# Kernel tuning notes

Hardware: AMD Instinct MI355X
Metric: run time of the kernel (lower is better)

The kernel has to match this reference:

```python
import jax, jax.numpy as jnp
import numpy as np
import math

FILT_LEN = 10  # all Farras / dual filters are 10-tap
INV_SQRT2 = 1.0 / math.sqrt(2.0)

# Farras first-stage analysis filters (fs_farras), shape [tree(2), lo/hi(2), 10]
_F = 0.08838834764832
_G = 0.01122679215254
_H = 0.69587998903400
FAF_NP = np.array([
    [[0.0, -_F, _F, _H, _H, _F, -_F, _G, _G, 0.0],
     [0.0, -_G, _G, _F, _F, -_H, _H, -_F, -_F, 0.0]],
    [[_G, _G, -_F, _F, _H, _H, _F, -_F, 0.0, 0.0],
     [0.0, 0.0, -_F, -_F, _H, -_H, _F, _F, _G, -_G]]], dtype=np.float32)
# Kingsbury Q-shift dual filters (duelfilt / dualfilt1), shape [tree(2), lo/hi(2), 10]
_A = 0.03516384
_B = 0.08832942
_C = 0.23389032
_D = 0.76027237
_E = 0.58751830
_K = 0.11430184
AF_NP = np.array([
    [[_A, 0.0, -_B, _C, _D, _E, 0.0, -_K, 0.0, 0.0],
     [0.0, 0.0, -_K, 0.0, _E, -_D, _C, _B, 0.0, -_A]],
    [[0.0, 0.0, -_K, 0.0, _E, _D, _C, -_B, 0.0, _A],
     [-_A, 0.0, _B, _C, -_D, _E, 0.0, -_K, 0.0, 0.0]]], dtype=np.float32)


def _afb_axis(x, lo_f, hi_f, axis):
    """1D circular analysis filter bank along spatial `axis` (1=rows, 2=cols).
    x: (B,H,W,C). Returns (lo, hi), each halved along `axis`.
    Math: x <- cshift(x,-L); y = downsample2(fullconv(x,f)); wrap-add first L taps.
    """
    N = x.shape[axis]
    L = FILT_LEN // 2
    C = x.shape[-1]
    x = jnp.roll(x, -L, axis=axis)

    def conv(f):
        kf = f[::-1].astype(x.dtype)  # lax does correlation -> flip for convolution
        if axis == 1:
            ker = jnp.tile(kf.reshape(FILT_LEN, 1, 1, 1), (1, 1, 1, C))
            pad = [(FILT_LEN - 1, FILT_LEN - 1), (0, 0)]
            strides = (2, 1)
        else:
            ker = jnp.tile(kf.reshape(1, FILT_LEN, 1, 1), (1, 1, 1, C))
            pad = [(0, 0), (FILT_LEN - 1, FILT_LEN - 1)]
            strides = (1, 2)
        return jax.lax.conv_general_dilated(
            x, ker, window_strides=strides, padding=pad,
            dimension_numbers=('NHWC', 'HWIO', 'NHWC'),
            feature_group_count=C)  # depthwise, per-channel identical filter

    def wrap(y):
        # y has N//2 + L samples along axis; fold periodic tail into head
        head = (jax.lax.slice_in_dim(y, 0, L, axis=axis)
                + jax.lax.slice_in_dim(y, N // 2, N // 2 + L, axis=axis))
        body = jax.lax.slice_in_dim(y, L, N // 2, axis=axis)
        return jnp.concatenate([head, body], axis=axis)

    return wrap(conv(lo_f)), wrap(conv(hi_f))


def afb2d(x, lo_row, hi_row, lo_col, hi_col):
    """2D separable analysis filter bank: returns (lo, [lohi, hilo, hihi])."""
    Lr, Hr = _afb_axis(x, lo_row, hi_row, axis=1)
    lo, w0 = _afb_axis(Lr, lo_col, hi_col, axis=2)
    w1, w2 = _afb_axis(Hr, lo_col, hi_col, axis=2)
    return lo, [w0, w1, w2]


def _add_sub(a, b):
    return (a + b) * INV_SQRT2, (a - b) * INV_SQRT2


def _dtcwt(x, Faf, af, level):
    x = x / 2
    w = [[[None, None] for _ in range(2)] for _ in range(level + 1)]
    for m in range(2):
        for n in range(2):
            lo, w[0][m][n] = afb2d(x, Faf[m, 0], Faf[m, 1], Faf[n, 0], Faf[n, 1])
            for j in range(1, level):
                lo, w[j][m][n] = afb2d(lo, af[m, 0], af[m, 1], af[n, 0], af[n, 1])
            w[level][m][n] = lo
    # combine dual trees into (approx) complex pairs
    for j in range(level):
        for s in range(3):
            w[j][0][0][s], w[j][1][1][s] = _add_sub(w[j][0][0][s], w[j][1][1][s])
            w[j][0][1][s], w[j][1][0][s] = _add_sub(w[j][0][1][s], w[j][1][0][s])
    # multiscale 2x2 tiling reassembly (concat=True path)
    wc = w
    for j in range(level - 1, 0, -1):
        for a in range(2):
            for b in range(2):
                wc[j][a][b] = jnp.concatenate([
                    jnp.concatenate([wc[j + 1][a][b], wc[j][a][b][0]], axis=2),
                    jnp.concatenate([wc[j][a][b][1], wc[j][a][b][2]], axis=2)], axis=1)
    tiles = []
    for a in range(2):
        for b in range(2):
            tiles.append(jnp.concatenate([
                jnp.concatenate([wc[1][a][b], wc[0][a][b][0]], axis=2),
                jnp.concatenate([wc[0][a][b][1], wc[0][a][b][2]], axis=2)], axis=1))
    w0, w1, w2, w3 = tiles
    return jnp.concatenate([jnp.concatenate([w0, w1], axis=2),
                            jnp.concatenate([w2, w3], axis=2)], axis=1)


def setup_inputs() -> dict:
    key = jax.random.key(0)
    x = jax.random.normal(key, (8, 512, 512, 3), dtype=jnp.float32)
    return {"x": x, "Faf": jnp.asarray(FAF_NP), "af": jnp.asarray(AF_NP), "level": 3}


def reference(x, Faf, af, level):
    return _dtcwt(x, Faf, af, int(level))
```

## Files before the change

kernel.cpp:

```cpp
#include <hip/hip_runtime.h>


#define FF 0.08838834764832f
#define GG 0.01122679215254f
#define HHc 0.69587998903400f
#define AAc 0.03516384f
#define BBc 0.08832942f
#define CCc 0.23389032f
#define DDc 0.76027237f
#define EEc 0.58751830f
#define KKc 0.11430184f

__device__ __constant__ float c_filt[2][2][2][10] = {
  {
    { {0.f,-FF, FF, HHc, HHc, FF,-FF, GG, GG, 0.f},
      {0.f,-GG, GG, FF, FF,-HHc, HHc,-FF,-FF, 0.f} },
    { {GG, GG,-FF, FF, HHc, HHc, FF,-FF, 0.f, 0.f},
      {0.f, 0.f,-FF,-FF, HHc,-HHc, FF, FF, GG,-GG} }
  },
  {
    { {AAc, 0.f,-BBc, CCc, DDc, EEc, 0.f,-KKc, 0.f, 0.f},
      {0.f, 0.f,-KKc, 0.f, EEc,-DDc, CCc, BBc, 0.f,-AAc} },
    { {0.f, 0.f,-KKc, 0.f, EEc, DDc, CCc,-BBc, 0.f, AAc},
      {-AAc, 0.f, BBc, CCc,-DDc, EEc, 0.f,-KKc, 0.f, 0.f} }
  }
};

__device__ __forceinline__ void cmb(float& a, float& b) {
  const float k = 0.70710678118654752440f;
  const float s = (a + b) * k, d = (a - b) * k;
  a = s; b = d;
}

__device__ __forceinline__ int swz4(int f4) { return f4 ^ ((f4 >> 3) & 7); }

template<int LVL, int N, int Ho, int Wo>
__global__ __launch_bounds__(256) void fused_level(
    const float* __restrict__ src,
    float* __restrict__ llout,
    float* __restrict__ out)
{
  constexpr int half = N / 2;
  constexpr int W2 = 2 * Wo + 8;
  constexpr int NF = (LVL == 0) ? 4 : 8;
  constexpr int ROWF = 3 * N;
  constexpr int FL = 3 * W2;
  constexpr int SIF4 = (3 * W2 * NF) / 4 + 4;
  constexpr size_t ZS = (size_t)8 * N * N * 3;
  constexpr size_t ZOUT = (size_t)8 * half * half * 3;
  __shared__ __align__(16) float inter[Ho * SIF4 * 4];

  const int jt = blockIdx.x, it = blockIdx.y, b = blockIdx.z;
  const int i0 = it * Ho, j0 = jt * Wo;
  const int tid = threadIdx.x;

  int base = (2 * j0 - 4) * 3;
  if (base < 0) base += ROWF;

  constexpr int I4 = FL / 4;
  for (int item = tid; item < Ho * I4; item += 256) {
    const int il = item / I4;
    const int q4 = (item - il * I4) * 4;
    int fg = base + q4;
    if (fg >= ROWF) fg -= ROWF;
    const int ig = i0 + il;
    float acc[NF][4];
#pragma unroll
    for (int f = 0; f < NF; ++f)
#pragma unroll
      for (int k = 0; k < 4; ++k) acc[f][k] = 0.f;

    if constexpr (LVL == 0) {
      const float* sp = src + (size_t)b * N * ROWF + fg;
#pragma unroll
      for (int t = 0; t < 10; ++t) {
        const int r = (2 * ig + 5 - t) & (N - 1);
        const float4 v = *(const float4*)(sp + (size_t)r * ROWF);
#pragma unroll
        for (int f = 0; f < 4; ++f) {
          const float fc = c_filt[0][f >> 1][f & 1][t];
          acc[f][0] += fc * v.x; acc[f][1] += fc * v.y;
          acc[f][2] += fc * v.z; acc[f][3] += fc * v.w;
        }
      }
#pragma unroll
      for (int f = 0; f < 4; ++f)
#pragma unroll
        for (int k = 0; k < 4; ++k) acc[f][k] *= 0.5f;
    } else {
#pragma unroll
      for (int z = 0; z < 4; ++z) {
        const int m = z >> 1;
        const float* sp = src + (size_t)z * ZS + (size_t)b * N * ROWF + fg;
#pragma unroll
        for (int t = 0; t < 10; ++t) {
          const int r = (2 * ig + 5 - t) & (N - 1);
          const float4 v = *(const float4*)(sp + (size_t)r * ROWF);
          const float fl = c_filt[1][m][0][t], fh = c_filt[1][m][1][t];
          acc[2 * z][0] += fl * v.x; acc[2 * z][1] += fl * v.y;
          acc[2 * z][2] += fl * v.z; acc[2 * z][3] += fl * v.w;
          acc[2 * z + 1][0] += fh * v.x; acc[2 * z + 1][1] += fh * v.y;
          acc[2 * z + 1][2] += fh * v.z; acc[2 * z + 1][3] += fh * v.w;
        }
      }
    }
#pragma unroll
    for (int k = 0; k < 4; ++k) {
      const int fq = q4 + k;
      if constexpr (NF == 4) {
        float4 w = make_float4(acc[0][k], acc[1][k], acc[2][k], acc[3][k]);
        *(float4*)&inter[(il * SIF4 + swz4(fq)) * 4] = w;
      } else {
        float4 w0 = make_float4(acc[0][k], acc[1][k], acc[2][k], acc[3][k]);
        float4 w1 = make_float4(acc[4][k], acc[5][k], acc[6][k], acc[7][k]);
        *(float4*)&inter[(il * SIF4 + swz4(2 * fq)) * 4] = w0;
        *(float4*)&inter[(il * SIF4 + swz4(2 * fq + 1)) * 4] = w1;
      }
    }
  }
  __syncthreads();

  if (tid < Ho * Wo) {
    const int il = tid / Wo, jl = tid - (tid / Wo) * Wo;
    float LL[4][3] = {}, LH[4][3] = {}, HL[4][3] = {}, HH[4][3] = {};
#pragma unroll
    for (int s = 0; s < 10; ++s) {
      const int wl = 2 * jl + 9 - s;
#pragma unroll
      for (int c = 0; c < 3; ++c) {
        if constexpr (LVL == 0) {
          const int f4 = wl * 3 + c;
          const float4 v = *(const float4*)&inter[(il * SIF4 + swz4(f4)) * 4];
          const float a0 = v.x, d0 = v.y, a1 = v.z, d1 = v.w;
#pragma unroll
          for (int n = 0; n < 2; ++n) {
            const float fl = c_filt[0][n][0][s], fh = c_filt[0][n][1][s];
            LL[n][c] += fl * a0; LH[n][c] += fh * a0;
            HL[n][c] += fl * d0; HH[n][c] += fh * d0;
            LL[2 + n][c] += fl * a1; LH[2 + n][c] += fh * a1;
            HL[2 + n][c] += fl * d1; HH[2 + n][c] += fh * d1;
          }
        } else {
          const int f4 = (wl * 3 + c) * 2;
          const float4 v0 = *(const float4*)&inter[(il * SIF4 + swz4(f4)) * 4];
          const float4 v1 = *(const float4*)&inter[(il * SIF4 + swz4(f4 + 1)) * 4];
          const float az[4] = {v0.x, v0.z, v1.x, v1.z};
          const float dz[4] = {v0.y, v0.w, v1.y, v1.w};
#pragma unroll
          for (int z = 0; z < 4; ++z) {
            const int n = z & 1;
            const float fl = c_filt[1][n][0][s], fh = c_filt[1][n][1][s];
            LL[z][c] += fl * az[z]; LH[z][c] += fh * az[z];
            HL[z][c] += fl * dz[z]; HH[z][c] += fh * dz[z];
          }
        }
      }
    }
#pragma unroll
    for (int c = 0; c < 3; ++c) {
      cmb(LH[0][c], LH[3][c]); cmb(LH[1][c], LH[2][c]);
      cmb(HL[0][c], HL[3][c]); cmb(HL[1][c], HL[2][c]);
      cmb(HH[0][c], HH[3][c]); cmb(HH[1][c], HH[2][c]);
    }
    const int ig = i0 + il, jg = j0 + jl;
    const size_t outB = (size_t)b * (1024u * 1024u * 3u);
#pragma unroll
    for (int z = 0; z < 4; ++z) {
      const int m = z >> 1, n = z & 1;
      const int r0 = m * 512, c0 = n * 512;
      float* pLL;
      if constexpr (LVL == 2)
        pLL = out + outB + ((size_t)(r0 + ig) * 1024 + (c0 + jg)) * 3;
      else
        pLL = llout + (size_t)z * ZOUT + (((size_t)b * half + ig) * half + jg) * 3;
      pLL[0] = LL[z][0]; pLL[1] = LL[z][1]; pLL[2] = LL[z][2];
      float* pLH = out + outB + ((size_t)(r0 + ig) * 1024 + (c0 + half + jg)) * 3;
      pLH[0] = LH[z][0]; pLH[1] = LH[z][1]; pLH[2] = LH[z][2];
      float* pHL = out + outB + ((size_t)(r0 + half + ig) * 1024 + (c0 + jg)) * 3;
      pHL[0] = HL[z][0]; pHL[1] = HL[z][1]; pHL[2] = HL[z][2];
      float* pHH = out + outB + ((size_t)(r0 + half + ig) * 1024 + (c0 + half + jg)) * 3;
      pHH[0] = HH[z][0]; pHH[1] = HH[z][1]; pHH[2] = HH[z][2];
    }
  }
}

extern "C" void kernel_launch(void* const* d_in, const int* in_sizes, int n_in,
                              void* d_out, int out_size, void* d_ws, size_t ws_size,
                              hipStream_t stream) {
  (void)in_sizes; (void)n_in; (void)out_size; (void)ws_size;
  const float* x = (const float*)d_in[0];
  float* out = (float*)d_out;
  float* LL1 = (float*)d_ws;
  float* LL2 = LL1 + 6291456;

  fused_level<0, 512, 8, 32><<<dim3(8, 32, 8), 256, 0, stream>>>(x, LL1, out);
  fused_level<1, 256, 8, 16><<<dim3(8, 16, 8), 256, 0, stream>>>(LL1, LL2, out);
  fused_level<2, 128, 8, 16><<<dim3(4, 8, 8), 256, 0, stream>>>(LL2, nullptr, out);
}
```

Measured before the change: 165.1 us.

## Merge three level kernels into one persistent cooperative kernel with grid syncs

Replaces the three per-level launches with a single cooperative persistent kernel. Each block loops over tiles for a level, and grid.sync separates the levels. The goal is to remove launch overhead and the tail gaps between dependent kernels. In exchange it caps occupancy at the cooperative grid size, which also fixes LDS at the maximum tile size for every level, and it adds grid-wide barrier costs. The old three-launch path is kept as a fallback.

```diff
diff --git a/kernel.cpp b/kernel.cpp
--- a/kernel.cpp
+++ b/kernel.cpp
@@ -1,4 +1,7 @@
 #include <hip/hip_runtime.h>
+#include <hip/hip_cooperative_groups.h>
+
+namespace cg = cooperative_groups;
 
 
 #define FF 0.08838834764832f
@@ -35,10 +38,12 @@
 __device__ __forceinline__ int swz4(int f4) { return f4 ^ ((f4 >> 3) & 7); }
 
 template<int LVL, int N, int Ho, int Wo>
-__global__ __launch_bounds__(256) void fused_level(
+__device__ __forceinline__ void tile_level(
+    const int jt, const int it, const int b,
     const float* __restrict__ src,
     float* __restrict__ llout,
-    float* __restrict__ out)
+    float* __restrict__ out,
+    float* __restrict__ inter)
 {
   constexpr int half = N / 2;
   constexpr int W2 = 2 * Wo + 8;
@@ -48,9 +53,7 @@
   constexpr int SIF4 = (3 * W2 * NF) / 4 + 4;
   constexpr size_t ZS = (size_t)8 * N * N * 3;
   constexpr size_t ZOUT = (size_t)8 * half * half * 3;
-  __shared__ __align__(16) float inter[Ho * SIF4 * 4];
-
-  const int jt = blockIdx.x, it = blockIdx.y, b = blockIdx.z;
+
   const int i0 = it * Ho, j0 = jt * Wo;
   const int tid = threadIdx.x;
 
@@ -184,6 +187,46 @@
   }
 }
 
+#define INTER_FLOATS 7808
+
+__global__ __launch_bounds__(256, 2) void dtcwt_all(
+    const float* __restrict__ x,
+    float* __restrict__ LL1,
+    float* __restrict__ LL2,
+    float* __restrict__ out)
+{
+  __shared__ __align__(16) float inter[INTER_FLOATS];
+  cg::grid_group grid = cg::this_grid();
+  const int gb = blockIdx.x;
+  const int G  = gridDim.x;
+
+  for (int t = gb; t < 2048; t += G) {
+    tile_level<0, 512, 8, 32>(t & 7, (t >> 3) & 31, t >> 8, x, LL1, out, inter);
+    __syncthreads();
+  }
+  grid.sync();
+  for (int t = gb; t < 1024; t += G) {
+    tile_level<1, 256, 8, 16>(t & 7, (t >> 3) & 15, t >> 7, LL1, LL2, out, inter);
+    __syncthreads();
+  }
+  grid.sync();
+  for (int t = gb; t < 256; t += G) {
+    tile_level<2, 128, 8, 16>(t & 3, (t >> 2) & 7, t >> 5, LL2, nullptr, out, inter);
+    __syncthreads();
+  }
+}
+
+template<int LVL, int N, int Ho, int Wo>
+__global__ __launch_bounds__(256) void fused_level(
+    const float* __restrict__ src,
+    float* __restrict__ llout,
+    float* __restrict__ out)
+{
+  __shared__ __align__(16) float inter[INTER_FLOATS];
+  tile_level<LVL, N, Ho, Wo>(blockIdx.x, blockIdx.y, blockIdx.z,
+                             src, llout, out, inter);
+}
+
 extern "C" void kernel_launch(void* const* d_in, const int* in_sizes, int n_in,
                               void* d_out, int out_size, void* d_ws, size_t ws_size,
                               hipStream_t stream) {
@@ -193,6 +236,33 @@
   float* LL1 = (float*)d_ws;
   float* LL2 = LL1 + 6291456;
 
+  static int coop_grid = -2;
+  if (coop_grid == -2) {
+    int dev = 0;
+    (void)hipGetDevice(&dev);
+    int has_coop = 0;
+    (void)hipDeviceGetAttribute(&has_coop, hipDeviceAttributeCooperativeLaunch, dev);
+    int nb = 0;
+    if (has_coop) {
+      if (hipOccupancyMaxActiveBlocksPerMultiprocessor(&nb, dtcwt_all, 256, 0)
+          != hipSuccess)
+        nb = 0;
+    }
+    int ncu = 0;
+    (void)hipDeviceGetAttribute(&ncu, hipDeviceAttributeMultiprocessorCount, dev);
+    if (ncu <= 0) ncu = 256;
+    coop_grid = (nb >= 1) ? nb * ncu : -1;
+    if (coop_grid > 2048) coop_grid = 2048;
+  }
+
+  if (coop_grid > 0) {
+    void* args[] = {(void*)&x, (void*)&LL1, (void*)&LL2, (void*)&out};
+    hipError_t e = hipLaunchCooperativeKernel(dtcwt_all, dim3(coop_grid),
+                                              dim3(256), args, 0u, stream);
+    if (e == hipSuccess) return;
+    coop_grid = -1;
+  }
+
   fused_level<0, 512, 8, 32><<<dim3(8, 32, 8), 256, 0, stream>>>(x, LL1, out);
   fused_level<1, 256, 8, 16><<<dim3(8, 16, 8), 256, 0, stream>>>(LL1, LL2, out);
   fused_level<2, 128, 8, 16><<<dim3(4, 8, 8), 256, 0, stream>>>(LL2, nullptr, out);
```

Result: slower. 283.3 us (+71.6%).
